# Kernel tuning notes

Measured on AMD Instinct MI355X. Metric: run time of the kernel, lower is better.

## Reference

```python
import jax, jax.numpy as jnp
import numpy as np

B, N, L, D, H = 2, 2048, 2048, 1024, 16
HD = D // H  # 64


def setup_inputs() -> dict:
    key = jax.random.key(0)
    ks = jax.random.split(key, 12)
    s = 0.02
    return {
        "x_q": jax.random.normal(ks[0], (B, N, D), jnp.float32),
        "x_kv": jax.random.normal(ks[1], (B, L, D), jnp.float32),
        "pad_mask": jax.random.randint(ks[2], (B, L), 0, 2) > 0,
        "wq": jax.random.normal(ks[3], (D, D), jnp.float32) * s,
        "bq": jnp.zeros((D,), jnp.float32),
        "wk": jax.random.normal(ks[4], (D, D), jnp.float32) * s,
        "bk": jnp.zeros((D,), jnp.float32),
        "wv": jax.random.normal(ks[5], (D, D), jnp.float32) * s,
        "bv": jnp.zeros((D,), jnp.float32),
        "wo": jax.random.normal(ks[6], (D, D), jnp.float32) * s,
        "bo": jnp.zeros((D,), jnp.float32),
    }


def reference(x_q, x_kv, pad_mask, wq, bq, wk, bk, wv, bv, wo, bo):
    scale = HD ** -0.5
    # projections: (B, S, D) -> (B, H, S, HD)
    def split_heads(x):
        return x.reshape(x.shape[0], x.shape[1], H, HD).transpose(0, 2, 1, 3)
    q = split_heads(x_q @ wq + bq) * scale
    k = split_heads(x_kv @ wk + bk)
    v = split_heads(x_kv @ wv + bv)
    attn = jnp.einsum('bhic,bhjc->bhij', q, k)  # (B, H, N, L)
    neg = -jnp.finfo(attn.dtype).max
    attn = jnp.where(pad_mask[:, None, None, :], neg, attn)
    attn = jax.nn.softmax(attn, axis=-1)
    o = jnp.einsum('bhij,bhjc->bhic', attn, v)  # (B, H, N, HD)
    o = o.transpose(0, 2, 1, 3).reshape(B, N, D)
    return o @ wo + bo
```

## Files before the change

### kernel.cpp

```cpp
#include <hip/hip_runtime.h>
#include <hip/hip_bf16.h>
#include <math.h>

typedef __bf16 bf16;
typedef __attribute__((ext_vector_type(8))) __bf16 bf16x8;
typedef __attribute__((ext_vector_type(4))) __bf16 bf16x4;
typedef __attribute__((ext_vector_type(4))) float floatx4;

#define BB 2
#define NN 2048
#define LL 2048
#define DD 1024
#define HH 16
#define HDD 64

#define QSCALE (0.125f * 1.44269504f)
#define PCLAMP 21.66f
#define MBIAS  (-100000.0f)

__device__ __forceinline__ void async16(const bf16* g, bf16* l) {
  __builtin_amdgcn_global_load_lds((const __attribute__((address_space(1))) void*)(g),
                                   (__attribute__((address_space(3))) void*)(l), 16, 0, 0);
}

__global__ void detect_mask_kernel(const unsigned* __restrict__ m, int* __restrict__ flag) {
  __shared__ int hasBig, hasFloat;
  if (threadIdx.x == 0) { hasBig = 0; hasFloat = 0; }
  __syncthreads();
  int big = 0, flt = 0;
  for (int idx = threadIdx.x; idx < 1024; idx += 256) {
    unsigned v = m[idx];
    if (v == 0x3F800000u) flt = 1;
    else if (v > 1u) big = 1;
  }
  if (big) atomicOr(&hasBig, 1);
  if (flt) atomicOr(&hasFloat, 1);
  __syncthreads();
  if (threadIdx.x == 0) *flag = hasFloat ? 2 : (hasBig ? 1 : 0);
}

__global__ __launch_bounds__(256) void convert2_kernel(
    const float* __restrict__ srcA, bf16* __restrict__ dstA,
    const float* __restrict__ srcB, bf16* __restrict__ dstB, int nb, int n)
{
  int gid = blockIdx.x;
  const float* s = srcA; bf16* d = dstA;
  if (gid >= nb) { s = srcB; d = dstB; gid -= nb; }
  int idx = (gid * 256 + threadIdx.x) * 8;
  if (idx >= n) return;
  floatx4 a = *(const floatx4*)&s[idx];
  floatx4 b = *(const floatx4*)&s[idx + 4];
  bf16x8 o;
#pragma unroll
  for (int e = 0; e < 4; e++) { o[e] = (bf16)a[e]; o[4 + e] = (bf16)b[e]; }
  *(bf16x8*)&d[idx] = o;
}

__global__ __launch_bounds__(256) void wtrans_kernel(
    const float* __restrict__ W0, const float* __restrict__ W1,
    const float* __restrict__ W2, const float* __restrict__ W3,
    bf16* __restrict__ T0, bf16* __restrict__ T1,
    bf16* __restrict__ T2, bf16* __restrict__ T3)
{
  __shared__ bf16 Tb[64][72];
  const int bid = blockIdx.x;
  const int which = bid >> 8;
  const float* W = which == 0 ? W0 : which == 1 ? W1 : which == 2 ? W2 : W3;
  bf16*       T = which == 0 ? T0 : which == 1 ? T1 : which == 2 ? T2 : T3;
  const int tile = bid & 255;
  const int k0 = (tile >> 4) * 64, n0 = (tile & 15) * 64;
  const int t = threadIdx.x;
  const int r = t >> 2;
  const int c = (t & 3) * 16;
  const float* Wr = W + (size_t)(k0 + r) * 1024 + n0 + c;
  floatx4 f0 = *(const floatx4*)(Wr + 0);
  floatx4 f1 = *(const floatx4*)(Wr + 4);
  floatx4 f2 = *(const floatx4*)(Wr + 8);
  floatx4 f3 = *(const floatx4*)(Wr + 12);
#pragma unroll
  for (int e = 0; e < 4; e++) {
    Tb[c + e][r]      = (bf16)f0[e];
    Tb[c + 4 + e][r]  = (bf16)f1[e];
    Tb[c + 8 + e][r]  = (bf16)f2[e];
    Tb[c + 12 + e][r] = (bf16)f3[e];
  }
  __syncthreads();
  bf16* Tr = T + (size_t)(n0 + r) * 1024 + k0 + c;
  *(bf16x8*)&Tr[0] = *(const bf16x8*)&Tb[r][c];
  *(bf16x8*)&Tr[8] = *(const bf16x8*)&Tb[r][c + 8];
}

template <typename TC>
__device__ __forceinline__ void gemm_body(
    int bx, const bf16* __restrict__ A, const bf16* __restrict__ Wt,
    const float* __restrict__ bias, TC* __restrict__ C, float scale, int transv)
{
  __shared__ bf16 As[128 * 64];
  __shared__ bf16 Bs[64 * 64];

  const int tm = bx >> 4, tn = bx & 15;
  const int m0 = tm * 128, n0 = tn * 64;
  const int t = threadIdx.x;
  const int w = t >> 6, l = t & 63;
  const int q = l >> 4, i = l & 15;
  const int wm = (w >> 1) * 64, wn = (w & 1) * 32;
  const int sr = t >> 3;
  const int sc = (t & 7) * 8;

  const floatx4 zero = {0.f, 0.f, 0.f, 0.f};
  floatx4 acc[4][2];
#pragma unroll
  for (int mi = 0; mi < 4; mi++)
#pragma unroll
    for (int ni = 0; ni < 2; ni++) acc[mi][ni] = zero;

  for (int k0 = 0; k0 < 1024; k0 += 64) {
    __syncthreads();
#pragma unroll
    for (int j = 0; j < 4; j++)
      async16(&A[(size_t)(m0 + j * 32 + sr) * 1024 + k0 + sc], &As[(j * 32 + sr) * 64 + sc]);
#pragma unroll
    for (int j = 0; j < 2; j++)
      async16(&Wt[(size_t)(n0 + j * 32 + sr) * 1024 + k0 + sc], &Bs[(j * 32 + sr) * 64 + sc]);
    __syncthreads();
#pragma unroll
    for (int ks = 0; ks < 2; ks++) {
      bf16x8 af[4], bfr[2];
#pragma unroll
      for (int mi = 0; mi < 4; mi++)
        af[mi] = *(const bf16x8*)&As[(wm + mi * 16 + i) * 64 + ks * 32 + q * 8];
#pragma unroll
      for (int ni = 0; ni < 2; ni++)
        bfr[ni] = *(const bf16x8*)&Bs[(wn + ni * 16 + i) * 64 + ks * 32 + q * 8];
#pragma unroll
      for (int mi = 0; mi < 4; mi++)
#pragma unroll
        for (int ni = 0; ni < 2; ni++)
          acc[mi][ni] = __builtin_amdgcn_mfma_f32_16x16x32_bf16(af[mi], bfr[ni], acc[mi][ni], 0, 0, 0);
    }
  }
#pragma unroll
  for (int ni = 0; ni < 2; ni++) {
    int col = n0 + wn + ni * 16 + i;
    float bv = bias[col];
#pragma unroll
    for (int mi = 0; mi < 4; mi++) {
      int row = m0 + wm + mi * 16 + q * 4;
      if (transv) {
        int bb = row >> 11, key = row & 2047;
        bf16x4 v4;
#pragma unroll
        for (int r = 0; r < 4; r++) v4[r] = (bf16)(acc[mi][ni][r] + bv);
        *(bf16x4*)&((bf16*)C)[(size_t)bb * (DD * (size_t)LL) + (size_t)col * LL + key] = v4;
      } else {
#pragma unroll
        for (int r = 0; r < 4; r++)
          C[(size_t)(row + r) * 1024 + col] = (TC)((acc[mi][ni][r] + bv) * scale);
      }
    }
  }
}

__global__ __launch_bounds__(256) void qkv_gemm(
    const bf16* __restrict__ Xq, const bf16* __restrict__ Xkv,
    const bf16* __restrict__ Wtq, const bf16* __restrict__ Wtk, const bf16* __restrict__ Wtv,
    const float* __restrict__ bq, const float* __restrict__ bk, const float* __restrict__ bv,
    bf16* __restrict__ Qp, bf16* __restrict__ Kp, bf16* __restrict__ VtG, int shift)
{
  const int bid = blockIdx.x;
  const int which = bid >> shift;
  const int bx = bid & ((1 << shift) - 1);
  if (which == 0)      gemm_body<bf16>(bx, Xq,  Wtq, bq, Qp,  QSCALE, 0);
  else if (which == 1) gemm_body<bf16>(bx, Xkv, Wtk, bk, Kp,  1.0f,   0);
  else                 gemm_body<bf16>(bx, Xkv, Wtv, bv, VtG, 1.0f,   1);
}

__global__ __launch_bounds__(256) void out_gemm(
    const bf16* __restrict__ A, const bf16* __restrict__ Wt,
    const float* __restrict__ bias, float* __restrict__ C)
{
  gemm_body<float>(blockIdx.x, A, Wt, bias, C, 1.0f, 0);
}

__global__ __launch_bounds__(256) void attn_kernel(
    const bf16* __restrict__ Q, const bf16* __restrict__ K,
    const bf16* __restrict__ Vt, const void* __restrict__ mask,
    const int* __restrict__ flag, bf16* __restrict__ O, int hbits, int mbase)
{
  __shared__ bf16 Ks[64][72];
  __shared__ bf16 Vs[64][72];
  __shared__ bf16 Ps[4][16][72];
  __shared__ float biasL[2048];

  const int bid = blockIdx.x;
  const int qt = bid >> hbits;
  const int hb = bid & ((1 << hbits) - 1);
  const int h  = (hbits == 5) ? (hb >> 1) : hb;
  const int b  = (hbits == 5) ? (hb & 1) : 0;
  const int t = threadIdx.x;
  const int w = t >> 6, lane = t & 63;
  const int q = lane >> 4, i = lane & 15;

  const int mode = *flag;
  const int mb = mbase + b;
  {
    const int base = t * 8;
    if (mode == 0) {
      const int* mm = ((const int*)mask) + mb * LL + base;
#pragma unroll
      for (int e = 0; e < 8; e++) biasL[base + e] = mm[e] ? MBIAS : 0.0f;
    } else if (mode == 1) {
      const unsigned char* mm = ((const unsigned char*)mask) + mb * LL + base;
#pragma unroll
      for (int e = 0; e < 8; e++) biasL[base + e] = mm[e] ? MBIAS : 0.0f;
    } else {
      const float* mm = ((const float*)mask) + mb * LL + base;
#pragma unroll
      for (int e = 0; e < 8; e++) biasL[base + e] = (mm[e] != 0.0f) ? MBIAS : 0.0f;
    }
  }

  const bf16* Qb = Q  + (size_t)b * (NN * DD) + h * HDD;
  const bf16* Kb = K  + (size_t)b * (LL * DD) + h * HDD;
  const bf16* Vb = Vt + (size_t)b * (DD * (size_t)LL) + (size_t)(h * HDD) * LL;

  const int qrow = qt * 64 + w * 16;
  bf16x8 qfrag[2];
#pragma unroll
  for (int ks = 0; ks < 2; ks++)
    qfrag[ks] = *(const bf16x8*)&Qb[(size_t)(qrow + i) * DD + ks * 32 + q * 8];

  const floatx4 zero = {0.f, 0.f, 0.f, 0.f};
  floatx4 oacc[4];
#pragma unroll
  for (int n = 0; n < 4; n++) oacc[n] = zero;
  float psum = 0.0f;

  const int ldr = t >> 3;
  const int ldc = (t & 7) * 8;

  bf16x8 pk0 = *(const bf16x8*)&Kb[(size_t)ldr * DD + ldc];
  bf16x8 pk1 = *(const bf16x8*)&Kb[(size_t)(ldr + 32) * DD + ldc];
  bf16x8 pv0 = *(const bf16x8*)&Vb[(size_t)ldr * LL + ldc];
  bf16x8 pv1 = *(const bf16x8*)&Vb[(size_t)(ldr + 32) * LL + ldc];

  for (int kt = 0; kt < LL; kt += 64) {
    __syncthreads();
    *(bf16x8*)&Ks[ldr][ldc]      = pk0;
    *(bf16x8*)&Ks[ldr + 32][ldc] = pk1;
    *(bf16x8*)&Vs[ldr][ldc]      = pv0;
    *(bf16x8*)&Vs[ldr + 32][ldc] = pv1;
    __syncthreads();

    {
      const int ktn = (kt + 64) & (LL - 1);
      pk0 = *(const bf16x8*)&Kb[(size_t)(ktn + ldr) * DD + ldc];
      pk1 = *(const bf16x8*)&Kb[(size_t)(ktn + ldr + 32) * DD + ldc];
      pv0 = *(const bf16x8*)&Vb[(size_t)ldr * LL + ktn + ldc];
      pv1 = *(const bf16x8*)&Vb[(size_t)(ldr + 32) * LL + ktn + ldc];
    }

#pragma unroll
    for (int n = 0; n < 4; n++) {
      floatx4 bv = *(const floatx4*)&biasL[kt + n * 16 + q * 4];
      floatx4 a = bv;
#pragma unroll
      for (int ks = 0; ks < 2; ks++) {
        bf16x8 kf = *(const bf16x8*)&Ks[n * 16 + i][ks * 32 + q * 8];
        a = __builtin_amdgcn_mfma_f32_16x16x32_bf16(kf, qfrag[ks], a, 0, 0, 0);
      }
      bf16x4 v4;
#pragma unroll
      for (int r = 0; r < 4; r++) {
        float p = __builtin_amdgcn_exp2f(fminf(a[r], PCLAMP));
        psum += p;
        v4[r] = (bf16)p;
      }
      *(bf16x4*)&Ps[w][i][n * 16 + q * 4] = v4;
    }
    bf16x8 pf[2];
#pragma unroll
    for (int ks = 0; ks < 2; ks++)
      pf[ks] = *(const bf16x8*)&Ps[w][i][ks * 32 + q * 8];
#pragma unroll
    for (int n = 0; n < 4; n++) {
#pragma unroll
      for (int ks = 0; ks < 2; ks++) {
        bf16x8 vf = *(const bf16x8*)&Vs[n * 16 + i][ks * 32 + q * 8];
        oacc[n] = __builtin_amdgcn_mfma_f32_16x16x32_bf16(vf, pf[ks], oacc[n], 0, 0, 0);
      }
    }
  }

  psum += __shfl_xor(psum, 16, 64);
  psum += __shfl_xor(psum, 32, 64);
  float inv = 1.0f / fmaxf(psum, 1e-30f);

  bf16* Ob = O + (size_t)b * (NN * DD) + h * HDD;
#pragma unroll
  for (int n = 0; n < 4; n++) {
    bf16x4 v4;
#pragma unroll
    for (int r = 0; r < 4; r++) v4[r] = (bf16)(oacc[n][r] * inv);
    *(bf16x4*)&Ob[(size_t)(qrow + i) * DD + n * 16 + q * 4] = v4;
  }
}

extern "C" void kernel_launch(void* const* d_in, const int* in_sizes, int n_in,
                              void* d_out, int out_size, void* d_ws, size_t ws_size,
                              hipStream_t stream)
{
  const float* x_q  = (const float*)d_in[0];
  const float* x_kv = (const float*)d_in[1];
  const void*  pad  = d_in[2];
  const float* wq = (const float*)d_in[3];
  const float* bq = (const float*)d_in[4];
  const float* wk = (const float*)d_in[5];
  const float* bk = (const float*)d_in[6];
  const float* wv = (const float*)d_in[7];
  const float* bv = (const float*)d_in[8];
  const float* wo = (const float*)d_in[9];
  const float* bo = (const float*)d_in[10];
  float* out = (float*)d_out;

  char* ws = (char*)d_ws;
  const size_t MB = (size_t)1 << 20;
  const size_t fullElems = (size_t)BB * NN * DD;
  const size_t batchElems = (size_t)NN * DD;

  int* flag = (int*)((char*)d_out + (size_t)out_size * sizeof(float) - 16);
  detect_mask_kernel<<<1, 256, 0, stream>>>((const unsigned*)pad, flag);

  if (ws_size >= 48 * MB) {
    bf16* Xqb  = (bf16*)(ws);
    bf16* Xkvb = (bf16*)(ws + 8 * MB);
    bf16* Wtq  = (bf16*)(ws + 16 * MB);
    bf16* Wtk  = (bf16*)(ws + 18 * MB);
    bf16* Wtv  = (bf16*)(ws + 20 * MB);
    bf16* Wto  = (bf16*)(ws + 22 * MB);
    bf16* Qp   = (bf16*)(ws + 24 * MB);
    bf16* Kp   = (bf16*)(ws + 32 * MB);
    bf16* VtG  = (bf16*)(ws + 40 * MB);
    bf16* Op   = Xqb;

    convert2_kernel<<<4096, 256, 0, stream>>>(x_q, Xqb, x_kv, Xkvb, 2048, (int)fullElems);
    wtrans_kernel<<<1024, 256, 0, stream>>>(wq, wk, wv, wo, Wtq, Wtk, Wtv, Wto);
    qkv_gemm<<<1536, 256, 0, stream>>>(Xqb, Xkvb, Wtq, Wtk, Wtv, bq, bk, bv, Qp, Kp, VtG, 9);
    attn_kernel<<<1024, 256, 0, stream>>>(Qp, Kp, VtG, pad, flag, Op, 5, 0);
    out_gemm<<<512, 256, 0, stream>>>(Op, Wto, bo, out);
  } else {
    bf16* Wtq  = (bf16*)(ws);
    bf16* Wtk  = (bf16*)(ws + 2 * MB);
    bf16* Wtv  = (bf16*)(ws + 4 * MB);
    bf16* Wto  = (bf16*)(ws + 6 * MB);
    bf16* Xqb  = (bf16*)(ws + 8 * MB);
    bf16* Xkvb = (bf16*)(ws + 12 * MB);
    bf16* Qp   = (bf16*)(ws + 16 * MB);
    bf16* Kp   = (bf16*)(ws + 20 * MB);
    bf16* VtG  = (bf16*)(ws + 24 * MB);
    bf16* Op   = Xqb;

    wtrans_kernel<<<1024, 256, 0, stream>>>(wq, wk, wv, wo, Wtq, Wtk, Wtv, Wto);
    for (int b = 0; b < BB; b++) {
      convert2_kernel<<<2048, 256, 0, stream>>>(x_q + b * batchElems, Xqb,
                                                x_kv + b * batchElems, Xkvb,
                                                1024, (int)batchElems);
      qkv_gemm<<<768, 256, 0, stream>>>(Xqb, Xkvb, Wtq, Wtk, Wtv, bq, bk, bv, Qp, Kp, VtG, 8);
      attn_kernel<<<512, 256, 0, stream>>>(Qp, Kp, VtG, pad, flag, Op, 4, b);
      out_gemm<<<256, 256, 0, stream>>>(Op, Wto, bo, out + b * batchElems);
    }
  }
}
```

Before: 244.1 us.

## Fuse prep kernels, use 32x32 MFMA QKV GEMM, precompute mask bias

Merges the mask detection, input conversion and weight transpose into one prep kernel that also writes a global float mask bias. The QKV GEMM switches to 128x128 tiles with 32x32x16 MFMA to raise data reuse. The attention kernel now prefetches bias from global memory per tile instead of building a 2048-entry LDS bias per block. This removes kernel launches and per-block mask decoding, at the cost of more registers in the GEMM and an extra global read stream in attention.

Measured after the change: 267.5 us. +9.6%, slower.

```diff
diff --git a/kernel.cpp b/kernel.cpp
--- a/kernel.cpp
+++ b/kernel.cpp
@@ -6,6 +6,7 @@
 typedef __attribute__((ext_vector_type(8))) __bf16 bf16x8;
 typedef __attribute__((ext_vector_type(4))) __bf16 bf16x4;
 typedef __attribute__((ext_vector_type(4))) float floatx4;
+typedef __attribute__((ext_vector_type(16))) float floatx16;
 
 #define BB 2
 #define NN 2048
@@ -23,81 +24,183 @@
                                    (__attribute__((address_space(3))) void*)(l), 16, 0, 0);
 }
 
-__global__ void detect_mask_kernel(const unsigned* __restrict__ m, int* __restrict__ flag) {
+__global__ __launch_bounds__(256) void prep_kernel(
+    const float* __restrict__ xq, const float* __restrict__ xkv,
+    bf16* __restrict__ Xqb, bf16* __restrict__ Xkvb, int nconv, int elemsEach,
+    const float* __restrict__ W0, const float* __restrict__ W1,
+    const float* __restrict__ W2, const float* __restrict__ W3,
+    bf16* __restrict__ T0, bf16* __restrict__ T1,
+    bf16* __restrict__ T2, bf16* __restrict__ T3,
+    const unsigned* __restrict__ mask, float* __restrict__ biasF)
+{
+  __shared__ bf16 Tb[64][72];
+  const int bid = blockIdx.x;
+  const int t = threadIdx.x;
+
+  if (bid < nconv) {
+    const int half = nconv >> 1;
+    const float* s = (bid < half) ? xq : xkv;
+    bf16* d = (bid < half) ? Xqb : Xkvb;
+    int gid = (bid < half) ? bid : bid - half;
+    int idx = (gid * 256 + t) * 8;
+    if (idx >= elemsEach) return;
+    floatx4 a = *(const floatx4*)&s[idx];
+    floatx4 b = *(const floatx4*)&s[idx + 4];
+    bf16x8 o;
+#pragma unroll
+    for (int e = 0; e < 4; e++) { o[e] = (bf16)a[e]; o[4 + e] = (bf16)b[e]; }
+    *(bf16x8*)&d[idx] = o;
+    return;
+  }
+  if (bid < nconv + 1024) {
+    const int wb = bid - nconv;
+    const int which = wb >> 8;
+    const float* W = which == 0 ? W0 : which == 1 ? W1 : which == 2 ? W2 : W3;
+    bf16*       T = which == 0 ? T0 : which == 1 ? T1 : which == 2 ? T2 : T3;
+    const int tile = wb & 255;
+    const int k0 = (tile >> 4) * 64, n0 = (tile & 15) * 64;
+    const int r = t >> 2;
+    const int c = (t & 3) * 16;
+    const float* Wr = W + (size_t)(k0 + r) * 1024 + n0 + c;
+    floatx4 f0 = *(const floatx4*)(Wr + 0);
+    floatx4 f1 = *(const floatx4*)(Wr + 4);
+    floatx4 f2 = *(const floatx4*)(Wr + 8);
+    floatx4 f3 = *(const floatx4*)(Wr + 12);
+#pragma unroll
+    for (int e = 0; e < 4; e++) {
+      Tb[c + e][r]      = (bf16)f0[e];
+      Tb[c + 4 + e][r]  = (bf16)f1[e];
+      Tb[c + 8 + e][r]  = (bf16)f2[e];
+      Tb[c + 12 + e][r] = (bf16)f3[e];
+    }
+    __syncthreads();
+    bf16* Tr = T + (size_t)(n0 + r) * 1024 + k0 + c;
+    *(bf16x8*)&Tr[0] = *(const bf16x8*)&Tb[r][c];
+    *(bf16x8*)&Tr[8] = *(const bf16x8*)&Tb[r][c + 8];
+    return;
+  }
   __shared__ int hasBig, hasFloat;
-  if (threadIdx.x == 0) { hasBig = 0; hasFloat = 0; }
+  if (t == 0) { hasBig = 0; hasFloat = 0; }
   __syncthreads();
   int big = 0, flt = 0;
-  for (int idx = threadIdx.x; idx < 1024; idx += 256) {
-    unsigned v = m[idx];
+  for (int idx = t; idx < 1024; idx += 256) {
+    unsigned v = mask[idx];
     if (v == 0x3F800000u) flt = 1;
     else if (v > 1u) big = 1;
   }
   if (big) atomicOr(&hasBig, 1);
   if (flt) atomicOr(&hasFloat, 1);
   __syncthreads();
-  if (threadIdx.x == 0) *flag = hasFloat ? 2 : (hasBig ? 1 : 0);
-}
-
-__global__ __launch_bounds__(256) void convert2_kernel(
-    const float* __restrict__ srcA, bf16* __restrict__ dstA,
-    const float* __restrict__ srcB, bf16* __restrict__ dstB, int nb, int n)
-{
-  int gid = blockIdx.x;
-  const float* s = srcA; bf16* d = dstA;
-  if (gid >= nb) { s = srcB; d = dstB; gid -= nb; }
-  int idx = (gid * 256 + threadIdx.x) * 8;
-  if (idx >= n) return;
-  floatx4 a = *(const floatx4*)&s[idx];
-  floatx4 b = *(const floatx4*)&s[idx + 4];
-  bf16x8 o;
-#pragma unroll
-  for (int e = 0; e < 4; e++) { o[e] = (bf16)a[e]; o[4 + e] = (bf16)b[e]; }
-  *(bf16x8*)&d[idx] = o;
-}
-
-__global__ __launch_bounds__(256) void wtrans_kernel(
-    const float* __restrict__ W0, const float* __restrict__ W1,
-    const float* __restrict__ W2, const float* __restrict__ W3,
-    bf16* __restrict__ T0, bf16* __restrict__ T1,
-    bf16* __restrict__ T2, bf16* __restrict__ T3)
-{
-  __shared__ bf16 Tb[64][72];
-  const int bid = blockIdx.x;
-  const int which = bid >> 8;
-  const float* W = which == 0 ? W0 : which == 1 ? W1 : which == 2 ? W2 : W3;
-  bf16*       T = which == 0 ? T0 : which == 1 ? T1 : which == 2 ? T2 : T3;
-  const int tile = bid & 255;
-  const int k0 = (tile >> 4) * 64, n0 = (tile & 15) * 64;
-  const int t = threadIdx.x;
-  const int r = t >> 2;
-  const int c = (t & 3) * 16;
-  const float* Wr = W + (size_t)(k0 + r) * 1024 + n0 + c;
-  floatx4 f0 = *(const floatx4*)(Wr + 0);
-  floatx4 f1 = *(const floatx4*)(Wr + 4);
-  floatx4 f2 = *(const floatx4*)(Wr + 8);
-  floatx4 f3 = *(const floatx4*)(Wr + 12);
-#pragma unroll
-  for (int e = 0; e < 4; e++) {
-    Tb[c + e][r]      = (bf16)f0[e];
-    Tb[c + 4 + e][r]  = (bf16)f1[e];
-    Tb[c + 8 + e][r]  = (bf16)f2[e];
-    Tb[c + 12 + e][r] = (bf16)f3[e];
-  }
-  __syncthreads();
-  bf16* Tr = T + (size_t)(n0 + r) * 1024 + k0 + c;
-  *(bf16x8*)&Tr[0] = *(const bf16x8*)&Tb[r][c];
-  *(bf16x8*)&Tr[8] = *(const bf16x8*)&Tb[r][c + 8];
+  const int mode = hasFloat ? 2 : (hasBig ? 1 : 0);
+  for (int k = t * 16; k < t * 16 + 16; k++) {
+    bool m;
+    if (mode == 0)      m = ((const int*)mask)[k] != 0;
+    else if (mode == 1) m = ((const unsigned char*)mask)[k] != 0;
+    else                m = ((const float*)mask)[k] != 0.0f;
+    biasF[k] = m ? MBIAS : 0.0f;
+  }
 }
 
 template <typename TC>
-__device__ __forceinline__ void gemm_body(
+__device__ __forceinline__ void gemm_body32(
     int bx, const bf16* __restrict__ A, const bf16* __restrict__ Wt,
     const float* __restrict__ bias, TC* __restrict__ C, float scale, int transv)
 {
   __shared__ bf16 As[128 * 64];
+  __shared__ bf16 Bs[128 * 64];
+
+  const int tm = bx >> 3, tn = bx & 7;
+  const int m0 = tm * 128, n0 = tn * 128;
+  const int t = threadIdx.x;
+  const int w = t >> 6, l = t & 63;
+  const int col = l & 31, half = l >> 5;
+  const int wm = (w >> 1) * 64, wn = (w & 1) * 64;
+  const int sr = t >> 3;
+  const int sc = (t & 7) * 8;
+
+  floatx16 acc[2][2];
+#pragma unroll
+  for (int mi = 0; mi < 2; mi++)
+#pragma unroll
+    for (int ni = 0; ni < 2; ni++)
+#pragma unroll
+      for (int e = 0; e < 16; e++) acc[mi][ni][e] = 0.0f;
+
+  for (int k0 = 0; k0 < 1024; k0 += 64) {
+    __syncthreads();
+#pragma unroll
+    for (int j = 0; j < 4; j++)
+      async16(&A[(size_t)(m0 + j * 32 + sr) * 1024 + k0 + sc], &As[(j * 32 + sr) * 64 + sc]);
+#pragma unroll
+    for (int j = 0; j < 4; j++)
+      async16(&Wt[(size_t)(n0 + j * 32 + sr) * 1024 + k0 + sc], &Bs[(j * 32 + sr) * 64 + sc]);
+    __syncthreads();
+#pragma unroll
+    for (int kk = 0; kk < 4; kk++) {
+      bf16x8 af[2], bfr[2];
+#pragma unroll
+      for (int mi = 0; mi < 2; mi++)
+        af[mi] = *(const bf16x8*)&As[(wm + mi * 32 + col) * 64 + kk * 16 + half * 8];
+#pragma unroll
+      for (int ni = 0; ni < 2; ni++)
+        bfr[ni] = *(const bf16x8*)&Bs[(wn + ni * 32 + col) * 64 + kk * 16 + half * 8];
+#pragma unroll
+      for (int mi = 0; mi < 2; mi++)
+#pragma unroll
+        for (int ni = 0; ni < 2; ni++)
+          acc[mi][ni] = __builtin_amdgcn_mfma_f32_32x32x16_bf16(af[mi], bfr[ni], acc[mi][ni], 0, 0, 0);
+    }
+  }
+#pragma unroll
+  for (int ni = 0; ni < 2; ni++) {
+    int colg = n0 + wn + ni * 32 + col;
+    float bv = bias[colg];
+#pragma unroll
+    for (int mi = 0; mi < 2; mi++) {
+      int rbase = m0 + wm + mi * 32 + half * 4;
+      if (transv) {
+#pragma unroll
+        for (int g = 0; g < 4; g++) {
+          int key0 = rbase + g * 8;
+          int bb = key0 >> 11, key = key0 & 2047;
+          bf16x4 v4;
+#pragma unroll
+          for (int r = 0; r < 4; r++) v4[r] = (bf16)(acc[mi][ni][g * 4 + r] + bv);
+          *(bf16x4*)&((bf16*)C)[(size_t)bb * (DD * (size_t)LL) + (size_t)colg * LL + key] = v4;
+        }
+      } else {
+#pragma unroll
+        for (int g = 0; g < 4; g++)
+#pragma unroll
+          for (int r = 0; r < 4; r++)
+            C[(size_t)(rbase + g * 8 + r) * 1024 + colg] = (TC)((acc[mi][ni][g * 4 + r] + bv) * scale);
+      }
+    }
+  }
+}
+
+__global__ __launch_bounds__(256) void qkv_gemm32(
+    const bf16* __restrict__ Xq, const bf16* __restrict__ Xkv,
+    const bf16* __restrict__ Wtq, const bf16* __restrict__ Wtk, const bf16* __restrict__ Wtv,
+    const float* __restrict__ bq, const float* __restrict__ bk, const float* __restrict__ bv,
+    bf16* __restrict__ Qp, bf16* __restrict__ Kp, bf16* __restrict__ VtG, int shift)
+{
+  const int bid = blockIdx.x;
+  const int which = bid >> shift;
+  const int bx = bid & ((1 << shift) - 1);
+  if (which == 0)      gemm_body32<bf16>(bx, Xq,  Wtq, bq, Qp,  QSCALE, 0);
+  else if (which == 1) gemm_body32<bf16>(bx, Xkv, Wtk, bk, Kp,  1.0f,   0);
+  else                 gemm_body32<bf16>(bx, Xkv, Wtv, bv, VtG, 1.0f,   1);
+}
+
+__global__ __launch_bounds__(256) void out_gemm(
+    const bf16* __restrict__ A, const bf16* __restrict__ Wt,
+    const float* __restrict__ bias, float* __restrict__ C)
+{
+  __shared__ bf16 As[128 * 64];
   __shared__ bf16 Bs[64 * 64];
 
+  const int bx = blockIdx.x;
   const int tm = bx >> 4, tn = bx & 15;
   const int m0 = tm * 128, n0 = tn * 64;
   const int t = threadIdx.x;
@@ -146,51 +249,21 @@
 #pragma unroll
     for (int mi = 0; mi < 4; mi++) {
       int row = m0 + wm + mi * 16 + q * 4;
-      if (transv) {
-        int bb = row >> 11, key = row & 2047;
-        bf16x4 v4;
-#pragma unroll
-        for (int r = 0; r < 4; r++) v4[r] = (bf16)(acc[mi][ni][r] + bv);
-        *(bf16x4*)&((bf16*)C)[(size_t)bb * (DD * (size_t)LL) + (size_t)col * LL + key] = v4;
-      } else {
-#pragma unroll
-        for (int r = 0; r < 4; r++)
-          C[(size_t)(row + r) * 1024 + col] = (TC)((acc[mi][ni][r] + bv) * scale);
-      }
-    }
-  }
-}
-
-__global__ __launch_bounds__(256) void qkv_gemm(
-    const bf16* __restrict__ Xq, const bf16* __restrict__ Xkv,
-    const bf16* __restrict__ Wtq, const bf16* __restrict__ Wtk, const bf16* __restrict__ Wtv,
-    const float* __restrict__ bq, const float* __restrict__ bk, const float* __restrict__ bv,
-    bf16* __restrict__ Qp, bf16* __restrict__ Kp, bf16* __restrict__ VtG, int shift)
-{
-  const int bid = blockIdx.x;
-  const int which = bid >> shift;
-  const int bx = bid & ((1 << shift) - 1);
-  if (which == 0)      gemm_body<bf16>(bx, Xq,  Wtq, bq, Qp,  QSCALE, 0);
-  else if (which == 1) gemm_body<bf16>(bx, Xkv, Wtk, bk, Kp,  1.0f,   0);
-  else                 gemm_body<bf16>(bx, Xkv, Wtv, bv, VtG, 1.0f,   1);
-}
-
-__global__ __launch_bounds__(256) void out_gemm(
-    const bf16* __restrict__ A, const bf16* __restrict__ Wt,
-    const float* __restrict__ bias, float* __restrict__ C)
-{
-  gemm_body<float>(blockIdx.x, A, Wt, bias, C, 1.0f, 0);
+#pragma unroll
+      for (int r = 0; r < 4; r++)
+        C[(size_t)(row + r) * 1024 + col] = acc[mi][ni][r] + bv;
+    }
+  }
 }
 
 __global__ __launch_bounds__(256) void attn_kernel(
     const bf16* __restrict__ Q, const bf16* __restrict__ K,
-    const bf16* __restrict__ Vt, const void* __restrict__ mask,
-    const int* __restrict__ flag, bf16* __restrict__ O, int hbits, int mbase)
+    const bf16* __restrict__ Vt, const float* __restrict__ biasF,
+    bf16* __restrict__ O, int hbits)
 {
   __shared__ bf16 Ks[64][72];
   __shared__ bf16 Vs[64][72];
   __shared__ bf16 Ps[4][16][72];
-  __shared__ float biasL[2048];
 
   const int bid = blockIdx.x;
   const int qt = bid >> hbits;
@@ -201,28 +274,10 @@
   const int w = t >> 6, lane = t & 63;
   const int q = lane >> 4, i = lane & 15;
 
-  const int mode = *flag;
-  const int mb = mbase + b;
-  {
-    const int base = t * 8;
-    if (mode == 0) {
-      const int* mm = ((const int*)mask) + mb * LL + base;
-#pragma unroll
-      for (int e = 0; e < 8; e++) biasL[base + e] = mm[e] ? MBIAS : 0.0f;
-    } else if (mode == 1) {
-      const unsigned char* mm = ((const unsigned char*)mask) + mb * LL + base;
-#pragma unroll
-      for (int e = 0; e < 8; e++) biasL[base + e] = mm[e] ? MBIAS : 0.0f;
-    } else {
-      const float* mm = ((const float*)mask) + mb * LL + base;
-#pragma unroll
-      for (int e = 0; e < 8; e++) biasL[base + e] = (mm[e] != 0.0f) ? MBIAS : 0.0f;
-    }
-  }
-
   const bf16* Qb = Q  + (size_t)b * (NN * DD) + h * HDD;
   const bf16* Kb = K  + (size_t)b * (LL * DD) + h * HDD;
   const bf16* Vb = Vt + (size_t)b * (DD * (size_t)LL) + (size_t)(h * HDD) * LL;
+  const float* biasFb = biasF + b * LL;
 
   const int qrow = qt * 64 + w * 16;
   bf16x8 qfrag[2];
@@ -230,10 +285,12 @@
   for (int ks = 0; ks < 2; ks++)
     qfrag[ks] = *(const bf16x8*)&Qb[(size_t)(qrow + i) * DD + ks * 32 + q * 8];
 
-  const floatx4 zero = {0.f, 0.f, 0.f, 0.f};
   floatx4 oacc[4];
 #pragma unroll
-  for (int n = 0; n < 4; n++) oacc[n] = zero;
+  for (int n = 0; n < 4; n++) {
+#pragma unroll
+    for (int r = 0; r < 4; r++) oacc[n][r] = 0.0f;
+  }
   float psum = 0.0f;
 
   const int ldr = t >> 3;
@@ -243,6 +300,10 @@
   bf16x8 pk1 = *(const bf16x8*)&Kb[(size_t)(ldr + 32) * DD + ldc];
   bf16x8 pv0 = *(const bf16x8*)&Vb[(size_t)ldr * LL + ldc];
   bf16x8 pv1 = *(const bf16x8*)&Vb[(size_t)(ldr + 32) * LL + ldc];
+  floatx4 pb[4];
+#pragma unroll
+  for (int n = 0; n < 4; n++)
+    pb[n] = *(const floatx4*)&biasFb[n * 16 + q * 4];
 
   for (int kt = 0; kt < LL; kt += 64) {
     __syncthreads();
@@ -262,8 +323,7 @@
 
 #pragma unroll
     for (int n = 0; n < 4; n++) {
-      floatx4 bv = *(const floatx4*)&biasL[kt + n * 16 + q * 4];
-      floatx4 a = bv;
+      floatx4 a = pb[n];
 #pragma unroll
       for (int ks = 0; ks < 2; ks++) {
         bf16x8 kf = *(const bf16x8*)&Ks[n * 16 + i][ks * 32 + q * 8];
@@ -277,6 +337,12 @@
         v4[r] = (bf16)p;
       }
       *(bf16x4*)&Ps[w][i][n * 16 + q * 4] = v4;
+    }
+    {
+      const int ktn = (kt + 64) & (LL - 1);
+#pragma unroll
+      for (int n = 0; n < 4; n++)
+        pb[n] = *(const floatx4*)&biasFb[ktn + n * 16 + q * 4];
     }
     bf16x8 pf[2];
 #pragma unroll
@@ -328,45 +394,50 @@
   const size_t fullElems = (size_t)BB * NN * DD;
   const size_t batchElems = (size_t)NN * DD;
 
-  int* flag = (int*)((char*)d_out + (size_t)out_size * sizeof(float) - 16);
-  detect_mask_kernel<<<1, 256, 0, stream>>>((const unsigned*)pad, flag);
-
-  if (ws_size >= 48 * MB) {
-    bf16* Xqb  = (bf16*)(ws);
-    bf16* Xkvb = (bf16*)(ws + 8 * MB);
-    bf16* Wtq  = (bf16*)(ws + 16 * MB);
-    bf16* Wtk  = (bf16*)(ws + 18 * MB);
-    bf16* Wtv  = (bf16*)(ws + 20 * MB);
-    bf16* Wto  = (bf16*)(ws + 22 * MB);
-    bf16* Qp   = (bf16*)(ws + 24 * MB);
-    bf16* Kp   = (bf16*)(ws + 32 * MB);
-    bf16* VtG  = (bf16*)(ws + 40 * MB);
-    bf16* Op   = Xqb;
-
-    convert2_kernel<<<4096, 256, 0, stream>>>(x_q, Xqb, x_kv, Xkvb, 2048, (int)fullElems);
-    wtrans_kernel<<<1024, 256, 0, stream>>>(wq, wk, wv, wo, Wtq, Wtk, Wtv, Wto);
-    qkv_gemm<<<1536, 256, 0, stream>>>(Xqb, Xkvb, Wtq, Wtk, Wtv, bq, bk, bv, Qp, Kp, VtG, 9);
-    attn_kernel<<<1024, 256, 0, stream>>>(Qp, Kp, VtG, pad, flag, Op, 5, 0);
+  if (ws_size >= 49 * MB) {
+    bf16* Xqb   = (bf16*)(ws);
+    bf16* Xkvb  = (bf16*)(ws + 8 * MB);
+    bf16* Wtq   = (bf16*)(ws + 16 * MB);
+    bf16* Wtk   = (bf16*)(ws + 18 * MB);
+    bf16* Wtv   = (bf16*)(ws + 20 * MB);
+    bf16* Wto   = (bf16*)(ws + 22 * MB);
+    bf16* Qp    = (bf16*)(ws + 24 * MB);
+    bf16* Kp    = (bf16*)(ws + 32 * MB);
+    bf16* VtG   = (bf16*)(ws + 40 * MB);
+    float* biasF = (float*)(ws + 48 * MB);
+    bf16* Op    = Xqb;
+
+    prep_kernel<<<5121, 256, 0, stream>>>(x_q, x_kv, Xqb, Xkvb, 4096, (int)fullElems,
+                                          wq, wk, wv, wo, Wtq, Wtk, Wtv, Wto,
+                                          (const unsigned*)pad, biasF);
+    qkv_gemm32<<<768, 256, 0, stream>>>(Xqb, Xkvb, Wtq, Wtk, Wtv, bq, bk, bv, Qp, Kp, VtG, 8);
+    attn_kernel<<<1024, 256, 0, stream>>>(Qp, Kp, VtG, biasF, Op, 5);
     out_gemm<<<512, 256, 0, stream>>>(Op, Wto, bo, out);
   } else {
-    bf16* Wtq  = (bf16*)(ws);
-    bf16* Wtk  = (bf16*)(ws + 2 * MB);
-    bf16* Wtv  = (bf16*)(ws + 4 * MB);
-    bf16* Wto  = (bf16*)(ws + 6 * MB);
-    bf16* Xqb  = (bf16*)(ws + 8 * MB);
-    bf16* Xkvb = (bf16*)(ws + 12 * MB);
-    bf16* Qp   = (bf16*)(ws + 16 * MB);
-    bf16* Kp   = (bf16*)(ws + 20 * MB);
-    bf16* VtG  = (bf16*)(ws + 24 * MB);
-    bf16* Op   = Xqb;
-
-    wtrans_kernel<<<1024, 256, 0, stream>>>(wq, wk, wv, wo, Wtq, Wtk, Wtv, Wto);
+    bf16* Wtq   = (bf16*)(ws);
+    bf16* Wtk   = (bf16*)(ws + 2 * MB);
+    bf16* Wtv   = (bf16*)(ws + 4 * MB);
+    bf16* Wto   = (bf16*)(ws + 6 * MB);
+    bf16* Xqb   = (bf16*)(ws + 8 * MB);
+    bf16* Xkvb  = (bf16*)(ws + 12 * MB);
+    bf16* Qp    = (bf16*)(ws + 16 * MB);
+    bf16* Kp    = (bf16*)(ws + 20 * MB);
+    bf16* VtG   = (bf16*)(ws + 24 * MB);
+    float* biasF = (float*)(ws + 28 * MB);
+    bf16* Op    = Xqb;
+
     for (int b = 0; b < BB; b++) {
-      convert2_kernel<<<2048, 256, 0, stream>>>(x_q + b * batchElems, Xqb,
-                                                x_kv + b * batchElems, Xkvb,
-                                                1024, (int)batchElems);
-      qkv_gemm<<<768, 256, 0, stream>>>(Xqb, Xkvb, Wtq, Wtk, Wtv, bq, bk, bv, Qp, Kp, VtG, 8);
-      attn_kernel<<<512, 256, 0, stream>>>(Qp, Kp, VtG, pad, flag, Op, 4, b);
+      if (b == 0)
+        prep_kernel<<<3073, 256, 0, stream>>>(x_q, x_kv, Xqb, Xkvb, 2048, (int)batchElems,
+                                              wq, wk, wv, wo, Wtq, Wtk, Wtv, Wto,
+                                              (const unsigned*)pad, biasF);
+      else
+        prep_kernel<<<2048, 256, 0, stream>>>(x_q + b * batchElems, x_kv + b * batchElems,
+                                              Xqb, Xkvb, 2048, (int)batchElems,
+                                              wq, wk, wv, wo, Wtq, Wtk, Wtv, Wto,
+                                              (const unsigned*)pad, biasF);
+      qkv_gemm32<<<384, 256, 0, stream>>>(Xqb, Xkvb, Wtq, Wtk, Wtv, bq, bk, bv, Qp, Kp, VtG, 7);
+      attn_kernel<<<512, 256, 0, stream>>>(Qp, Kp, VtG, biasF + b * LL, Op, 4);
       out_gemm<<<256, 256, 0, stream>>>(Op, Wto, bo, out + b * batchElems);
     }
   }
```
